# Kernel optimization log

Hardware: AMD Instinct MI355X
Metric: run time of the kernel (lower is better)

Reference implementation:

```python
import jax, jax.numpy as jnp
import numpy as np

GH = 256       # GRU hidden size
VOCAB = 1000
MAX_EP = 150
NPREV = NCURR = NNEXT = 64


def _gru_scan(emb, h0, wih, whh, bih, bhh):
    # torch nn.GRU single-layer math, scanned over the token axis
    H = h0.shape[0]
    def step(h, x_t):
        gi = wih @ x_t + bih            # [3H]
        gh = whh @ h + bhh              # [3H]
        r = jax.nn.sigmoid(gi[:H] + gh[:H])
        z = jax.nn.sigmoid(gi[H:2 * H] + gh[H:2 * H])
        n = jnp.tanh(gi[2 * H:] + r * gh[2 * H:])
        hn = (1.0 - z) * n + z * h
        return hn, hn
    _, hs = jax.lax.scan(step, h0, emb)
    return hs                            # [L, H]


def _conv(x, w, b, s):
    y = jax.lax.conv_general_dilated(x, w, (s, s), 'VALID',
                                     dimension_numbers=('NCHW', 'OIHW', 'NCHW'))
    return y + b[None, :, None, None]


def setup_inputs():
    key = jax.random.key(0)
    ks = jax.random.split(key, 48)
    f32 = jnp.float32
    def W(i, shape, s=0.05):
        return (jax.random.normal(ks[i], shape) * s).astype(f32)
    inp = dict(
        x=jax.random.normal(ks[0], (1, 3, 124, 124), f32),
        hx=jax.random.normal(ks[1], (1, 256), f32),
        cx=jax.random.normal(ks[2], (1, 256), f32),
        conv1_w=W(3, (128, 3, 8, 8)), conv1_b=jnp.zeros((128,), f32),
        conv2_w=W(4, (64, 128, 4, 4)), conv2_b=jnp.zeros((64,), f32),
        conv3_w=W(5, (64, 64, 4, 4)), conv3_b=jnp.zeros((64,), f32),
        emb_w=W(6, (VOCAB, 32), 1.0),
        gru_f_wih=W(7, (3 * GH, 32)), gru_f_whh=W(8, (3 * GH, GH)),
        gru_f_bih=jnp.zeros((3 * GH,), f32), gru_f_bhh=jnp.zeros((3 * GH,), f32),
        gru_b_wih=W(9, (3 * GH, 32)), gru_b_whh=W(10, (3 * GH, GH)),
        gru_b_bih=jnp.zeros((3 * GH,), f32), gru_b_bhh=jnp.zeros((3 * GH,), f32),
        time_emb_w=W(11, (MAX_EP + 1, 32), 1.0),
        temp_emb_w=W(12, (2, 32), 1.0),
        img_emb_w=W(13, (256, 64 * 6 * 6)), img_emb_b=jnp.zeros((256,), f32),
        attn_key_w=W(14, (256, 256 * 3)), attn_key_b=jnp.zeros((256,), f32),
        bilinear_A=W(15, (1, 256, 544)), bilinear_b=jnp.zeros((1,), f32),
        reduce_w=W(16, (128, 544)), reduce_b=jnp.zeros((128,), f32),
        gate_w=W(17, (64, 640)), gate_b=jnp.zeros((64,), f32),
        lin_w=W(18, (256, 64 * 6 * 6)), lin_b=jnp.zeros((256,), f32),
        lstm_wih=W(19, (1024, 256)), lstm_whh=W(20, (1024, 256)),
        lstm_bih=jnp.zeros((1024,), f32), lstm_bhh=jnp.zeros((1024,), f32),
        critic_w=W(21, (1, 288)), critic_b=jnp.zeros((1,), f32),
        actor_w=W(22, (4, 288)), actor_b=jnp.zeros((4,), f32),
        prev_inst=jax.random.randint(ks[23], (1, NPREV), 0, VOCAB),
        curr_inst=jax.random.randint(ks[24], (1, NCURR), 0, VOCAB),
        next_inst=jax.random.randint(ks[25], (1, NNEXT), 0, VOCAB),
        tx=jax.random.randint(ks[26], (1,), 0, MAX_EP + 1),
    )
    return inp


def reference(x, hx, cx, conv1_w, conv1_b, conv2_w, conv2_b, conv3_w, conv3_b,
              emb_w, gru_f_wih, gru_f_whh, gru_f_bih, gru_f_bhh,
              gru_b_wih, gru_b_whh, gru_b_bih, gru_b_bhh,
              time_emb_w, temp_emb_w, img_emb_w, img_emb_b,
              attn_key_w, attn_key_b, bilinear_A, bilinear_b,
              reduce_w, reduce_b, gate_w, gate_b, lin_w, lin_b,
              lstm_wih, lstm_whh, lstm_bih, lstm_bhh,
              critic_w, critic_b, actor_w, actor_b,
              prev_inst, curr_inst, next_inst, tx):
    np_, nc, nn_ = prev_inst.shape[1], curr_inst.shape[1], next_inst.shape[1]
    all_inst = jnp.concatenate([prev_inst, curr_inst, next_inst], axis=1)[0]  # [L]
    L = all_inst.shape[0]

    # CNN encoder
    h = jax.nn.relu(_conv(x, conv1_w, conv1_b, 4))
    h = jax.nn.relu(_conv(h, conv2_w, conv2_b, 2))
    x_img = jax.nn.relu(_conv(h, conv3_w, conv3_b, 2))       # [1,64,6,6]

    # token-looped GRUs -> single lax.scan each (note: original runs gru_b
    # over the SAME forward order then reverses the hidden list; replicated)
    emb = emb_w[all_inst]                                    # [L,32]
    h0 = jnp.zeros((GH,), emb.dtype)
    hs_f = _gru_scan(emb, h0, gru_f_wih, gru_f_whh, gru_f_bih, gru_f_bhh)
    hs_b = _gru_scan(emb, h0, gru_b_wih, gru_b_whh, gru_b_bih, gru_b_bhh)[::-1]
    curr_instr_rep = jnp.concatenate([hs_f[np_ + nc - 1], hs_b[np_]])[None]  # [1,512]
    ir_f = jnp.concatenate([hs_f[:np_], hs_f[L - nn_:]], axis=0)             # [M,256]
    ir_b = jnp.concatenate([hs_b[:np_], hs_b[L - nn_:]], axis=0)
    temp_tok = jnp.concatenate([jnp.zeros((np_,), jnp.int32), jnp.ones((nn_,), jnp.int32)])
    instr_rep = jnp.concatenate([ir_f, ir_b, temp_emb_w[temp_tok]], axis=1)  # [M,544]

    # bilinear attention over prev/next token states
    image_emb = x_img.reshape(1, -1) @ img_emb_w.T + img_emb_b               # [1,256]
    attn_key = jnp.concatenate([curr_instr_rep, image_emb], 1) @ attn_key_w.T + attn_key_b
    scores = jnp.einsum('k,okv,mv->mo', attn_key[0], bilinear_A, instr_rep) + bilinear_b  # [M,1]
    w = jax.nn.softmax(scores, axis=0)
    instr_sum = (instr_rep * w).sum(0, keepdims=True)                        # [1,544]

    # gating of image features
    gating = instr_sum @ reduce_w.T + reduce_b                               # [1,128]
    gate_key = jax.nn.sigmoid(jnp.concatenate([curr_instr_rep, gating], 1) @ gate_w.T + gate_b)  # [1,64]
    xg = (x_img * gate_key[:, :, None, None]).reshape(1, -1)
    z = jax.nn.relu(xg @ lin_w.T + lin_b)                                    # [1,256]

    # LSTMCell (torch gate order i,f,g,o)
    gates = z @ lstm_wih.T + lstm_bih + hx @ lstm_whh.T + lstm_bhh           # [1,1024]
    i, f, g, o = jnp.split(gates, 4, axis=1)
    cx2 = jax.nn.sigmoid(f) * cx + jax.nn.sigmoid(i) * jnp.tanh(g)
    hx2 = jax.nn.sigmoid(o) * jnp.tanh(cx2)

    feat = jnp.concatenate([hx2, time_emb_w[tx].reshape(-1, 32)], axis=1)    # [1,288]
    critic = feat @ critic_w.T + critic_b                                    # [1,1]
    actor = feat @ actor_w.T + actor_b                                       # [1,4]
    return critic, actor, hx2, cx2
```

## Files before the change

### kernel.cpp

```cpp
#include <hip/hip_runtime.h>
#include <hip/hip_bf16.h>

__device__ __forceinline__ float bf2f(unsigned short u) {
    unsigned int v = ((unsigned int)u) << 16;
    return __builtin_bit_cast(float, v);
}
__device__ __forceinline__ float sigm(float x) { return 1.0f / (1.0f + expf(-x)); }
__device__ __forceinline__ float san(float v) {
    return (v == v && fabsf(v) < 1e20f) ? v : 12345.0f;
}
__device__ __forceinline__ void wrout(void* out, int i, float v, int f32out) {
    if (f32out) ((float*)out)[i] = v;
    else ((__hip_bfloat16*)out)[i] = __float2bfloat16(v);
}
__device__ __forceinline__ int dot4(int a, int b, int c) {
#if __has_builtin(__builtin_amdgcn_sdot4)
    return __builtin_amdgcn_sdot4(a, b, c, false);
#else
    int d;
    asm("v_dot4_i32_i8 %0, %1, %2, %3" : "=v"(d) : "v"(a), "v"(b), "v"(c));
    return d;
#endif
}
__device__ __forceinline__ float fexp2(float x) {
#if __has_builtin(__builtin_amdgcn_exp2f)
    return __builtin_amdgcn_exp2f(x);
#else
    return exp2f(x);
#endif
}
__device__ __forceinline__ float frcp(float x) {
#if __has_builtin(__builtin_amdgcn_rcpf)
    return __builtin_amdgcn_rcpf(x);
#else
    return 1.0f / x;
#endif
}
__device__ __forceinline__ float fsigm(float x) {
    return frcp(1.0f + fexp2(x * -1.44269504f));
}
__device__ __forceinline__ float ftanh(float x) {
    float t = fexp2(x * 2.88539008f);
    return 1.0f - 2.0f * frcp(t + 1.0f);
}
__device__ __forceinline__ float wave_red(float acc) {
#pragma unroll
    for (int off = 32; off >= 1; off >>= 1) acc += __shfl_down(acc, off);
    return acc;
}
__device__ __forceinline__ int dpp_xor1(int a) {
    return __builtin_amdgcn_mov_dpp(a, 0xB1, 0xF, 0xF, true);
}
__device__ __forceinline__ int dpp_xor2(int a) {
    return __builtin_amdgcn_mov_dpp(a, 0x4E, 0xF, 0xF, true);
}
__device__ __forceinline__ int qsum4(int a) {
    a += dpp_xor1(a);
    a += dpp_xor2(a);
    return a;
}

struct CanonArgs {
    const void* ptr[40];
    int start[41];
    int size[40];
};

__global__ void k_flag1000(void* out) {
    if (threadIdx.x == 0) ((unsigned int*)out)[0] = 0x447A0000u;
}

__global__ void k_detect_tokens(const void* x, int nx,
                                const int* __restrict__ prev, const int* __restrict__ curr,
                                const int* __restrict__ nxt, const int* __restrict__ tx,
                                float* __restrict__ flags, int* __restrict__ toks) {
    __shared__ float sm[256];
    __shared__ int sInt64;
    int tid = threadIdx.x;
    const unsigned short* xs = (const unsigned short*)x;
    float mx = 0.0f;
    for (int i = tid; i < nx; i += 256) {
        float f = bf2f(xs[i]);
        float a = (f == f) ? fabsf(f) : 1e30f;
        mx = fmaxf(mx, a);
    }
    sm[tid] = mx;
    __syncthreads();
    for (int s = 128; s >= 1; s >>= 1) {
        if (tid < s) sm[tid] = fmaxf(sm[tid], sm[tid + s]);
        __syncthreads();
    }
    if (tid == 0) {
        flags[0] = (sm[0] > 100.0f) ? 1.0f : 0.0f;
        int anyOdd = 0;
        for (int k = 0; k < 32; ++k) anyOdd |= curr[2 * k + 1];
        int i64 = (anyOdd == 0) ? 1 : 0;
        flags[1] = (float)i64;
        sInt64 = i64;
    }
    __syncthreads();
    int stride = sInt64 ? 2 : 1;
    if (tid < 192) {
        const int* src = (tid < 64) ? prev : ((tid < 128) ? curr : nxt);
        int v = src[(tid & 63) * stride];
        toks[tid] = min(max(v, 0), 999);
    }
    if (tid == 0) toks[192] = min(max(tx[0], 0), 150);
}

__global__ void k_convert(CanonArgs a, const float* __restrict__ flags,
                          float* __restrict__ C) {
    int base = blockIdx.x << 10;
    int t = 0;
    while (t < 39 && base >= a.start[t + 1]) ++t;
    int local = base - a.start[t] + (threadIdx.x << 2);
    int sz = a.size[t];
    float4 v = make_float4(0.0f, 0.0f, 0.0f, 0.0f);
    int f32in = (flags[0] != 0.0f);
    if (local + 3 < sz) {
        if (f32in) {
            v = *(const float4*)((const float*)a.ptr[t] + local);
        } else {
            uint2 u = *(const uint2*)((const unsigned short*)a.ptr[t] + local);
            v.x = bf2f((unsigned short)(u.x & 0xffff));
            v.y = bf2f((unsigned short)(u.x >> 16));
            v.z = bf2f((unsigned short)(u.y & 0xffff));
            v.w = bf2f((unsigned short)(u.y >> 16));
        }
    } else if (local < sz) {
        float tmp[4] = {0.0f, 0.0f, 0.0f, 0.0f};
        for (int q = 0; q < 4 && local + q < sz; ++q) {
            if (f32in) tmp[q] = ((const float*)a.ptr[t])[local + q];
            else tmp[q] = bf2f(((const unsigned short*)a.ptr[t])[local + q]);
        }
        v = make_float4(tmp[0], tmp[1], tmp[2], tmp[3]);
    }
    *(float4*)(C + base + (threadIdx.x << 2)) = v;
}

__global__ void k_conv1(const float* __restrict__ x, const float* __restrict__ w,
                        const float* __restrict__ b, float* __restrict__ out) {
    int idx = blockIdx.x * 256 + threadIdx.x;
    int oc = idx / 900;
    int rem = idx - oc * 900;
    int oh = rem / 30;
    int ow = rem - oh * 30;
    float acc = b[oc];
    for (int ic = 0; ic < 3; ++ic) {
        int xb = ic * 15376 + (oh * 4) * 124 + ow * 4;
        int wb = oc * 192 + ic * 64;
#pragma unroll
        for (int kh = 0; kh < 8; ++kh) {
            const float2* xr = (const float2*)(x + xb + kh * 124);
            const float2* wr = (const float2*)(w + wb + kh * 8);
#pragma unroll
            for (int p = 0; p < 4; ++p) {
                float2 xv = xr[p];
                float2 wv = wr[p];
                acc += xv.x * wv.x + xv.y * wv.y;
            }
        }
    }
    out[idx] = fmaxf(acc, 0.0f);
}

__global__ void k_conv2(const float* __restrict__ in, const float* __restrict__ w,
                        const float* __restrict__ b, float* __restrict__ out) {
    int wid = (blockIdx.x * 256 + threadIdx.x) >> 6;
    int lane = threadIdx.x & 63;
    int oc = wid / 196;
    int rem = wid - oc * 196;
    int oh = rem / 14, ow = rem - oh * 14;
    float acc = 0.0f;
#pragma unroll 8
    for (int i = 0; i < 32; ++i) {
        int e = lane + (i << 6);
        int ic = e >> 4, k = e & 15, kh = k >> 2, kw = k & 3;
        acc += in[ic * 900 + (oh * 2 + kh) * 30 + ow * 2 + kw] * w[oc * 2048 + e];
    }
    acc = wave_red(acc);
    if (lane == 0) out[wid] = fmaxf(acc + b[oc], 0.0f);
}

__global__ void k_conv3(const float* __restrict__ in, const float* __restrict__ w,
                        const float* __restrict__ b, float* __restrict__ out) {
    int wid = (blockIdx.x * 256 + threadIdx.x) >> 6;
    int lane = threadIdx.x & 63;
    int oc = wid / 36;
    int rem = wid - oc * 36;
    int oh = rem / 6, ow = rem - oh * 6;
    float acc = 0.0f;
#pragma unroll
    for (int i = 0; i < 16; ++i) {
        int e = lane + (i << 6);
        int ic = e >> 4, k = e & 15, kh = k >> 2, kw = k & 3;
        acc += in[ic * 196 + (oh * 2 + kh) * 14 + ow * 2 + kw] * w[oc * 1024 + e];
    }
    acc = wave_red(acc);
    if (lane == 0) out[wid] = fmaxf(acc + b[oc], 0.0f);
}

__global__ void k_imgemb(const float* __restrict__ ximg, const float* __restrict__ w,
                         const float* __restrict__ b, float* __restrict__ out) {
    int j = blockIdx.x;
    int t = threadIdx.x;
    const float* wr = w + j * 2304;
    float acc = 0.0f;
    for (int k = t; k < 2304; k += 64) acc += wr[k] * ximg[k];
    acc = wave_red(acc);
    if (t == 0) out[j] = acc + b[j];
}

__global__ void k_gi(const int* __restrict__ toks, const float* __restrict__ emb,
                     const float* __restrict__ wih_f, const float* __restrict__ bih_f,
                     const float* __restrict__ bhh_f,
                     const float* __restrict__ wih_b, const float* __restrict__ bih_b,
                     const float* __restrict__ bhh_b,
                     float* __restrict__ gi) {
    int t = blockIdx.y;
    int gru = blockIdx.z;
    int j = blockIdx.x * 256 + threadIdx.x;
    __shared__ float e[32];
    int tok = toks[t];
    if (threadIdx.x < 32) e[threadIdx.x] = emb[tok * 32 + threadIdx.x];
    __syncthreads();
    const float* wih = gru ? wih_b : wih_f;
    const float* bih = gru ? bih_b : bih_f;
    const float* bhh = gru ? bhh_b : bhh_f;
    const float2* wr = (const float2*)(wih + j * 32);
    float acc = bih[j] + ((j < 512) ? bhh[j] : 0.0f);
#pragma unroll
    for (int k = 0; k < 16; ++k) {
        float2 wv = wr[k];
        acc += wv.x * e[2 * k] + wv.y * e[2 * k + 1];
    }
    gi[(gru * 192 + t) * 768 + j] = acc;
}

__global__ __launch_bounds__(512) void k_gru(
    const float* __restrict__ whh_f, const float* __restrict__ bhh_f,
    const float* __restrict__ whh_b, const float* __restrict__ bhh_b,
    const float* __restrict__ gi, float* __restrict__ hs) {
    extern __shared__ unsigned char smem[];
    unsigned int (*hq)[68] = (unsigned int (*)[68])smem;
    _Float16* hsl = (_Float16*)(smem + 1024);

    int gru = blockIdx.x;
    const float* whh = gru ? whh_b : whh_f;
    const float* bhh = gru ? bhh_b : bhh_f;
    const float* gib = gi + gru * 192 * 768;
    float* hso = hs + gru * 192 * 256;

    int t = threadIdx.x;
    int c = t & 3;
    int g = t >> 2;
    int j0 = g * 2;
    int d = c & 1;
    int jme = j0 + d;

    int wq[6][16];
    float inv[6];
#pragma unroll
    for (int rl = 0; rl < 6; ++rl) {
        int sect = rl >> 1, dd = rl & 1;
        int row = sect * 256 + j0 + dd;
        const float4* src4 = (const float4*)(whh + row * 256 + c * 64);
        float mx = 0.0f;
#pragma unroll
        for (int q = 0; q < 16; ++q) {
            float4 f = src4[q];
            mx = fmaxf(mx, fmaxf(fmaxf(fabsf(f.x), fabsf(f.y)), fmaxf(fabsf(f.z), fabsf(f.w))));
        }
        mx = fmaxf(mx, __shfl_xor(mx, 1));
        mx = fmaxf(mx, __shfl_xor(mx, 2));
        float scale = 127.0f / fmaxf(mx, 1e-20f);
        inv[rl] = mx * (1.0f / (127.0f * 127.0f));
#pragma unroll
        for (int q = 0; q < 16; ++q) {
            float4 f = src4[q];
            int p0 = (int)rintf(f.x * scale);
            int p1 = (int)rintf(f.y * scale);
            int p2 = (int)rintf(f.z * scale);
            int p3 = (int)rintf(f.w * scale);
            wq[rl][q] = (p0 & 0xff) | ((p1 & 0xff) << 8) | ((p2 & 0xff) << 16) | (p3 << 24);
        }
    }
    float bhhn = bhh[512 + jme];

    if (t < 68) {
        hq[0][t] = 0u;
        hq[1][t] = 0u;
    }
    __syncthreads();

    float hprev = 0.0f;
    float gir, giz, gin;
    {
        const float* gp = gib + jme;
        gir = gp[0]; giz = gp[256]; gin = gp[512];
    }

    for (int s = 0; s < 192; ++s) {
        int p = s & 1;
        float nir = 0.0f, niz = 0.0f, nin = 0.0f;
        if (s + 1 < 192) {
            const float* gp = gib + (s + 1) * 768 + jme;
            nir = gp[0]; niz = gp[256]; nin = gp[512];
        }
        int acc[6] = {0, 0, 0, 0, 0, 0};
        const uint4* hp = (const uint4*)&hq[p][c * 16];
#pragma unroll
        for (int blk = 0; blk < 4; ++blk) {
            uint4 hv = hp[blk];
#pragma unroll
            for (int rl = 0; rl < 6; ++rl) {
                acc[rl] = dot4(wq[rl][4 * blk + 0], (int)hv.x, acc[rl]);
                acc[rl] = dot4(wq[rl][4 * blk + 1], (int)hv.y, acc[rl]);
                acc[rl] = dot4(wq[rl][4 * blk + 2], (int)hv.z, acc[rl]);
                acc[rl] = dot4(wq[rl][4 * blk + 3], (int)hv.w, acc[rl]);
            }
        }
#pragma unroll
        for (int rl = 0; rl < 6; ++rl) acc[rl] = qsum4(acc[rl]);

        float ar = d ? (float)acc[1] * inv[1] : (float)acc[0] * inv[0];
        float az = d ? (float)acc[3] * inv[3] : (float)acc[2] * inv[2];
        float an = d ? (float)acc[5] * inv[5] : (float)acc[4] * inv[4];
        float r = fsigm(gir + ar);
        float z = fsigm(giz + az);
        float n = ftanh(gin + r * (an + bhhn));
        hprev = (1.0f - z) * n + z * hprev;

        int u = (int)(unsigned int)__builtin_bit_cast(unsigned short, (_Float16)hprev);
        int q = (int)rintf(hprev * 127.0f) & 0xff;
        int upk = u | (dpp_xor1(u) << 16);
        int qpk = q | ((dpp_xor1(q) & 0xff) << 8);
        if (c == 0) {
            ((unsigned int*)hsl)[s * 128 + g] = (unsigned int)upk;
            ((unsigned short*)&hq[1 - p][0])[g] = (unsigned short)qpk;
        }
        gir = nir; giz = niz; gin = nin;
        asm volatile("s_waitcnt lgkmcnt(0)" ::: "memory");
        __builtin_amdgcn_s_barrier();
        asm volatile("" ::: "memory");
    }

    const unsigned int* hsl32 = (const unsigned int*)hsl;
    for (int i = t; i < 24576; i += 512) {
        unsigned int u = hsl32[i];
        _Float16 lo = __builtin_bit_cast(_Float16, (unsigned short)(u & 0xffff));
        _Float16 hi = __builtin_bit_cast(_Float16, (unsigned short)(u >> 16));
        *(float2*)(hso + 2 * i) = make_float2((float)lo, (float)hi);
    }
}

__device__ __forceinline__ float ir_val(int m, int v, const float* hsf, const float* hsb,
                                        const float* temp_emb) {
    if (v < 256) { int r = (m < 64) ? m : 64 + m; return hsf[r * 256 + v]; }
    if (v < 512) { int r = (m < 64) ? 191 - m : 127 - m; return hsb[r * 256 + v - 256]; }
    return temp_emb[(m >= 64) * 32 + (v - 512)];
}

__global__ void k_attnkey(const float* __restrict__ hs, const float* __restrict__ imgemb,
                          const float* __restrict__ w, const float* __restrict__ b,
                          float* __restrict__ ak) {
    int j = blockIdx.x;
    int t = threadIdx.x;
    const float* hsf127 = hs + 127 * 256;
    const float* hsb127 = hs + 192 * 256 + 127 * 256;
    const float* wr = w + j * 768;
    float acc = 0.0f;
    for (int k = t; k < 768; k += 64) {
        float v = (k < 256) ? hsf127[k] : ((k < 512) ? hsb127[k - 256] : imgemb[k - 512]);
        acc += wr[k] * v;
    }
    acc = wave_red(acc);
    if (t == 0) ak[j] = acc + b[j];
}

__global__ void k_bilin(const float* __restrict__ A, const float* __restrict__ ak,
                        float* __restrict__ tmp) {
    int v = blockIdx.x;
    int t = threadIdx.x;
    float acc = 0.0f;
#pragma unroll
    for (int k = t; k < 256; k += 64) acc += A[k * 544 + v] * ak[k];
    acc = wave_red(acc);
    if (t == 0) tmp[v] = acc;
}

__global__ __launch_bounds__(1024) void k_attnmid(
    const float* __restrict__ hs, const float* __restrict__ temp_emb_w,
    const float* __restrict__ tmpv, const float* __restrict__ bb,
    const float* __restrict__ reduce_w, const float* __restrict__ reduce_b,
    const float* __restrict__ gate_w, const float* __restrict__ gate_b,
    float* __restrict__ gk) {
    const int tid = threadIdx.x;
    const float* hsf = hs;
    const float* hsb = hs + 192 * 256;
    __shared__ float stmp[544], ssc[128], ssum[544], sred[1024], sgating[128], scr[512];

    if (tid < 256) {
        scr[tid] = hsf[127 * 256 + tid];
        scr[256 + tid] = hsb[127 * 256 + tid];
    }
    if (tid < 544) stmp[tid] = tmpv[tid];
    __syncthreads();

    {
        int m = tid >> 3, q = tid & 7;
        float acc = 0.0f;
        for (int v = q * 68; v < q * 68 + 68; ++v) acc += stmp[v] * ir_val(m, v, hsf, hsb, temp_emb_w);
        sred[tid] = acc;
    }
    __syncthreads();
    if (tid < 128) {
        float acc = bb[0];
        for (int q = 0; q < 8; ++q) acc += sred[tid * 8 + q];
        ssc[tid] = acc;
        sred[tid] = acc;
    }
    __syncthreads();
#pragma unroll
    for (int s2 = 64; s2 >= 1; s2 >>= 1) {
        if (tid < s2) sred[tid] = fmaxf(sred[tid], sred[tid + s2]);
        __syncthreads();
    }
    float mx = sred[0];
    __syncthreads();
    if (tid < 128) {
        float e = expf(ssc[tid] - mx);
        ssc[tid] = e;
        sred[tid] = e;
    }
    __syncthreads();
#pragma unroll
    for (int s2 = 64; s2 >= 1; s2 >>= 1) {
        if (tid < s2) sred[tid] += sred[tid + s2];
        __syncthreads();
    }
    float inv = 1.0f / sred[0];
    __syncthreads();
    if (tid < 128) ssc[tid] *= inv;
    __syncthreads();

    if (tid < 544) {
        float acc = 0.0f;
        for (int m = 0; m < 128; ++m) acc += ssc[m] * ir_val(m, tid, hsf, hsb, temp_emb_w);
        ssum[tid] = acc;
    }
    __syncthreads();

    {
        int j = tid >> 3, q = tid & 7;
        const float2* wr = (const float2*)(reduce_w + j * 544 + q * 68);
        float acc = 0.0f;
        for (int k = 0; k < 34; ++k) {
            float2 wv = wr[k];
            acc += wv.x * ssum[q * 68 + 2 * k] + wv.y * ssum[q * 68 + 2 * k + 1];
        }
        sred[tid] = acc;
    }
    __syncthreads();
    if (tid < 128) {
        float acc = reduce_b[tid];
        for (int q = 0; q < 8; ++q) acc += sred[tid * 8 + q];
        sgating[tid] = acc;
    }
    __syncthreads();

    {
        int j = tid >> 4, q = tid & 15;
        const float2* wr = (const float2*)(gate_w + j * 640 + q * 40);
        float acc = 0.0f;
        for (int k = 0; k < 20; ++k) {
            float2 wv = wr[k];
            int v0 = q * 40 + 2 * k;
            float a0 = (v0 < 512) ? scr[v0] : sgating[v0 - 512];
            float a1 = (v0 + 1 < 512) ? scr[v0 + 1] : sgating[v0 + 1 - 512];
            acc += wv.x * a0 + wv.y * a1;
        }
        sred[tid] = acc;
    }
    __syncthreads();
    if (tid < 64) {
        float acc = gate_b[tid];
        for (int q = 0; q < 16; ++q) acc += sred[tid * 16 + q];
        gk[tid] = sigm(acc);
    }
}

__global__ void k_lin(const float* __restrict__ ximg, const float* __restrict__ gk,
                      const float* __restrict__ w, const float* __restrict__ b,
                      float* __restrict__ z) {
    int j = blockIdx.x;
    int t = threadIdx.x;
    __shared__ float sgk[64];
    if (t < 64) sgk[t] = gk[t];
    __syncthreads();
    const float* wr = w + j * 2304;
    float acc = 0.0f;
    for (int k = t; k < 2304; k += 64) acc += wr[k] * ximg[k] * sgk[k / 36];
    acc = wave_red(acc);
    if (t == 0) z[j] = fmaxf(acc + b[j], 0.0f);
}

__global__ void k_lstm(const float* __restrict__ z, const float* __restrict__ hx,
                       const float* __restrict__ wih, const float* __restrict__ whh,
                       const float* __restrict__ bih, const float* __restrict__ bhh,
                       float* __restrict__ sg) {
    int j = blockIdx.x;
    int t = threadIdx.x;
    const float* wi = wih + j * 256;
    const float* wh = whh + j * 256;
    float acc = 0.0f;
#pragma unroll
    for (int k = t; k < 256; k += 64) acc += wi[k] * z[k] + wh[k] * hx[k];
    acc = wave_red(acc);
    if (t == 0) sg[j] = acc + bih[j] + bhh[j];
}

__global__ __launch_bounds__(1024) void k_final(
    const float* __restrict__ sgg, const float* __restrict__ cx,
    const float* __restrict__ time_emb_w, const int* __restrict__ toks,
    const float* __restrict__ critic_w, const float* __restrict__ critic_b,
    const float* __restrict__ actor_w, const float* __restrict__ actor_b,
    const float* __restrict__ flags, void* __restrict__ out) {
    const int tid = threadIdx.x;
    __shared__ float sfeat[288], shx2[256], scx2[256], stmp[544], sred[1024];

    if (tid < 256) {
        float ii = sgg[tid], ff = sgg[256 + tid], gg = sgg[512 + tid], oo = sgg[768 + tid];
        float c2 = sigm(ff) * cx[tid] + sigm(ii) * tanhf(gg);
        float h2 = sigm(oo) * tanhf(c2);
        scx2[tid] = c2;
        shx2[tid] = h2;
        sfeat[tid] = h2;
    }
    if (tid < 32) sfeat[256 + tid] = time_emb_w[toks[192] * 32 + tid];
    __syncthreads();

    if (tid < 512) stmp[tid] = (tid < 288) ? critic_w[tid] * sfeat[tid] : 0.0f;
    {
        int a = tid >> 8, k = tid & 255;
        float pa = actor_w[a * 288 + k] * sfeat[k];
        if (k < 32) pa += actor_w[a * 288 + 256 + k] * sfeat[256 + k];
        sred[tid] = pa;
    }
    __syncthreads();
#pragma unroll
    for (int s2 = 256; s2 >= 1; s2 >>= 1) {
        if (tid < s2) stmp[tid] += stmp[tid + s2];
        int k = tid & 255;
        if (s2 <= 128 && k < s2) sred[tid] += sred[tid + s2];
        __syncthreads();
    }

    int f32out = (flags[0] != 0.0f) ? 1 : 0;
    if (tid == 0) wrout(out, 0, san(stmp[0] + critic_b[0]), f32out);
    if (tid < 4) wrout(out, 1 + tid, san(sred[tid * 256] + actor_b[tid]), f32out);
    if (tid < 256) {
        wrout(out, 5 + tid, san(shx2[tid]), f32out);
        wrout(out, 261 + tid, san(scx2[tid]), f32out);
    }
}

extern "C" void kernel_launch(void* const* d_in, const int* in_sizes, int n_in,
                              void* d_out, int out_size, void* d_ws, size_t ws_size,
                              hipStream_t stream) {
    if (n_in != 44) return;

    CanonArgs ca;
    int acc = 0;
    for (int i = 0; i < 40; ++i) {
        ca.ptr[i] = d_in[i];
        ca.start[i] = acc;
        ca.size[i] = in_sizes[i];
        acc += (in_sizes[i] + 1023) & ~1023;
    }
    ca.start[40] = acc;
    const int T = acc;

    float* ws     = (float*)d_ws;
    float* flags  = ws;
    int*   toks   = (int*)(ws + 64);
    float* imgemb = ws + 320;
    float* C      = ws + 640;
    float* gi     = C + T;
    float* hs     = gi + 294912;
    float* aux    = hs + 98304;
    float* ak     = aux;
    float* tmpv   = aux + 256;
    float* gk     = aux + 928;
    float* zv     = aux + 992;
    float* sg     = aux + 1248;
    float* h1     = gi;
    float* h2     = h1 + 115200;
    float* ximg   = h2 + 12544;

    size_t need = (size_t)(640 + T + 294912 + 98304 + 2272) * 4;
    if (ws_size < need) {
        k_flag1000<<<1, 64, 0, stream>>>(d_out);
        return;
    }

    const int* prev = (const int*)d_in[40];
    const int* curr = (const int*)d_in[41];
    const int* nxt  = (const int*)d_in[42];
    const int* tx   = (const int*)d_in[43];

    k_detect_tokens<<<1, 256, 0, stream>>>(d_in[0], in_sizes[0], prev, curr, nxt, tx,
                                           flags, toks);
    k_convert<<<T >> 10, 256, 0, stream>>>(ca, flags, C);

#define CP(i) (C + ca.start[i])
    k_gi<<<dim3(3, 192, 2), 256, 0, stream>>>(toks, CP(9),
                                              CP(10), CP(12), CP(13),
                                              CP(14), CP(16), CP(17), gi);
    k_gru<<<2, 512, 99328, stream>>>(CP(11), CP(13), CP(15), CP(17), gi, hs);
    k_conv1<<<450, 256, 0, stream>>>(CP(0), CP(3), CP(4), h1);
    k_conv2<<<3136, 256, 0, stream>>>(h1, CP(5), CP(6), h2);
    k_conv3<<<576, 256, 0, stream>>>(h2, CP(7), CP(8), ximg);
    k_imgemb<<<256, 64, 0, stream>>>(ximg, CP(20), CP(21), imgemb);
    k_attnkey<<<256, 64, 0, stream>>>(hs, imgemb, CP(22), CP(23), ak);
    k_bilin<<<544, 64, 0, stream>>>(CP(24), ak, tmpv);
    k_attnmid<<<1, 1024, 0, stream>>>(hs, CP(19), tmpv, CP(25),
                                      CP(26), CP(27), CP(28), CP(29), gk);
    k_lin<<<256, 64, 0, stream>>>(ximg, gk, CP(30), CP(31), zv);
    k_lstm<<<1024, 64, 0, stream>>>(zv, CP(1), CP(32), CP(33), CP(34), CP(35), sg);
    k_final<<<1, 1024, 0, stream>>>(sg, CP(2), CP(18), toks,
                                    CP(36), CP(37), CP(38), CP(39), flags, d_out);
#undef CP
}
```

Measured before the change: 523.4 us.

## Split GRU recurrent dot across 8 lanes with 1024 threads and store hs directly

The GRU recurrence kernel now runs 1024 threads per direction, and each group of 8 lanes splits the 256-wide hidden dot product. This halves the serial int8 dot4 chain per timestep, at the cost of one extra DPP half-mirror reduction step and a barrier across twice as many waves. The fp16 LDS staging buffer and the final copy-out loop are gone. Each step instead writes fp32 hidden states straight to global memory, which also removes the large dynamic shared allocation.

```diff
diff --git a/kernel.cpp b/kernel.cpp
--- a/kernel.cpp
+++ b/kernel.cpp
@@ -54,9 +54,13 @@
 __device__ __forceinline__ int dpp_xor2(int a) {
     return __builtin_amdgcn_mov_dpp(a, 0x4E, 0xF, 0xF, true);
 }
-__device__ __forceinline__ int qsum4(int a) {
+__device__ __forceinline__ int dpp_hmirror(int a) {
+    return __builtin_amdgcn_mov_dpp(a, 0x141, 0xF, 0xF, true);
+}
+__device__ __forceinline__ int gsum8(int a) {
     a += dpp_xor1(a);
     a += dpp_xor2(a);
+    a += dpp_hmirror(a);
     return a;
 }
 
@@ -237,13 +241,11 @@
     gi[(gru * 192 + t) * 768 + j] = acc;
 }
 
-__global__ __launch_bounds__(512) void k_gru(
+__global__ __launch_bounds__(1024, 4) void k_gru(
     const float* __restrict__ whh_f, const float* __restrict__ bhh_f,
     const float* __restrict__ whh_b, const float* __restrict__ bhh_b,
     const float* __restrict__ gi, float* __restrict__ hs) {
-    extern __shared__ unsigned char smem[];
-    unsigned int (*hq)[68] = (unsigned int (*)[68])smem;
-    _Float16* hsl = (_Float16*)(smem + 1024);
+    __shared__ unsigned int hq[2][72];
 
     int gru = blockIdx.x;
     const float* whh = gru ? whh_b : whh_f;
@@ -252,45 +254,47 @@
     float* hso = hs + gru * 192 * 256;
 
     int t = threadIdx.x;
-    int c = t & 3;
-    int g = t >> 2;
+    int c = t & 7;
+    int g = t >> 3;
     int j0 = g * 2;
     int d = c & 1;
     int jme = j0 + d;
 
-    int wq[6][16];
-    float inv[6];
+    int wq[6][8];
+    float inv6[6];
 #pragma unroll
     for (int rl = 0; rl < 6; ++rl) {
         int sect = rl >> 1, dd = rl & 1;
         int row = sect * 256 + j0 + dd;
-        const float4* src4 = (const float4*)(whh + row * 256 + c * 64);
+        const float4* src4 = (const float4*)(whh + row * 256 + c * 32);
+        float4 f[8];
         float mx = 0.0f;
 #pragma unroll
-        for (int q = 0; q < 16; ++q) {
-            float4 f = src4[q];
-            mx = fmaxf(mx, fmaxf(fmaxf(fabsf(f.x), fabsf(f.y)), fmaxf(fabsf(f.z), fabsf(f.w))));
+        for (int q = 0; q < 8; ++q) {
+            f[q] = src4[q];
+            mx = fmaxf(mx, fmaxf(fmaxf(fabsf(f[q].x), fabsf(f[q].y)),
+                                 fmaxf(fabsf(f[q].z), fabsf(f[q].w))));
         }
         mx = fmaxf(mx, __shfl_xor(mx, 1));
         mx = fmaxf(mx, __shfl_xor(mx, 2));
+        mx = fmaxf(mx, __shfl_xor(mx, 4));
         float scale = 127.0f / fmaxf(mx, 1e-20f);
-        inv[rl] = mx * (1.0f / (127.0f * 127.0f));
-#pragma unroll
-        for (int q = 0; q < 16; ++q) {
-            float4 f = src4[q];
-            int p0 = (int)rintf(f.x * scale);
-            int p1 = (int)rintf(f.y * scale);
-            int p2 = (int)rintf(f.z * scale);
-            int p3 = (int)rintf(f.w * scale);
+        inv6[rl] = mx * (1.0f / (127.0f * 127.0f));
+#pragma unroll
+        for (int q = 0; q < 8; ++q) {
+            int p0 = (int)rintf(f[q].x * scale);
+            int p1 = (int)rintf(f[q].y * scale);
+            int p2 = (int)rintf(f[q].z * scale);
+            int p3 = (int)rintf(f[q].w * scale);
             wq[rl][q] = (p0 & 0xff) | ((p1 & 0xff) << 8) | ((p2 & 0xff) << 16) | (p3 << 24);
         }
     }
+    float invR = d ? inv6[1] : inv6[0];
+    float invZ = d ? inv6[3] : inv6[2];
+    float invN = d ? inv6[5] : inv6[4];
     float bhhn = bhh[512 + jme];
 
-    if (t < 68) {
-        hq[0][t] = 0u;
-        hq[1][t] = 0u;
-    }
+    if (t < 144) ((unsigned int*)hq)[t] = 0u;
     __syncthreads();
 
     float hprev = 0.0f;
@@ -308,49 +312,48 @@
             nir = gp[0]; niz = gp[256]; nin = gp[512];
         }
         int acc[6] = {0, 0, 0, 0, 0, 0};
-        const uint4* hp = (const uint4*)&hq[p][c * 16];
-#pragma unroll
-        for (int blk = 0; blk < 4; ++blk) {
-            uint4 hv = hp[blk];
-#pragma unroll
-            for (int rl = 0; rl < 6; ++rl) {
-                acc[rl] = dot4(wq[rl][4 * blk + 0], (int)hv.x, acc[rl]);
-                acc[rl] = dot4(wq[rl][4 * blk + 1], (int)hv.y, acc[rl]);
-                acc[rl] = dot4(wq[rl][4 * blk + 2], (int)hv.z, acc[rl]);
-                acc[rl] = dot4(wq[rl][4 * blk + 3], (int)hv.w, acc[rl]);
-            }
-        }
-#pragma unroll
-        for (int rl = 0; rl < 6; ++rl) acc[rl] = qsum4(acc[rl]);
-
-        float ar = d ? (float)acc[1] * inv[1] : (float)acc[0] * inv[0];
-        float az = d ? (float)acc[3] * inv[3] : (float)acc[2] * inv[2];
-        float an = d ? (float)acc[5] * inv[5] : (float)acc[4] * inv[4];
+        const uint4* hp = (const uint4*)&hq[p][c * 8];
+        uint4 ha = hp[0];
+        uint4 hb = hp[1];
+#pragma unroll
+        for (int rl = 0; rl < 6; ++rl) {
+            acc[rl] = dot4(wq[rl][0], (int)ha.x, acc[rl]);
+            acc[rl] = dot4(wq[rl][1], (int)ha.y, acc[rl]);
+            acc[rl] = dot4(wq[rl][2], (int)ha.z, acc[rl]);
+            acc[rl] = dot4(wq[rl][3], (int)ha.w, acc[rl]);
+            acc[rl] = dot4(wq[rl][4], (int)hb.x, acc[rl]);
+            acc[rl] = dot4(wq[rl][5], (int)hb.y, acc[rl]);
+            acc[rl] = dot4(wq[rl][6], (int)hb.z, acc[rl]);
+            acc[rl] = dot4(wq[rl][7], (int)hb.w, acc[rl]);
+        }
+#pragma unroll
+        for (int rl = 0; rl < 6; ++rl) acc[rl] = gsum8(acc[rl]);
+
+        int ai_r = d ? acc[1] : acc[0];
+        int ai_z = d ? acc[3] : acc[2];
+        int ai_n = d ? acc[5] : acc[4];
+        float ar = (float)ai_r * invR;
+        float az = (float)ai_z * invZ;
+        float an = (float)ai_n * invN;
         float r = fsigm(gir + ar);
         float z = fsigm(giz + az);
         float n = ftanh(gin + r * (an + bhhn));
-        hprev = (1.0f - z) * n + z * hprev;
-
-        int u = (int)(unsigned int)__builtin_bit_cast(unsigned short, (_Float16)hprev);
+        hprev = z * (hprev - n) + n;
+
+        int hbits = __builtin_bit_cast(int, hprev);
+        int hpart = dpp_xor1(hbits);
+        if (c == 0) {
+            *(float2*)(hso + s * 256 + j0) =
+                make_float2(hprev, __builtin_bit_cast(float, hpart));
+        }
         int q = (int)rintf(hprev * 127.0f) & 0xff;
-        int upk = u | (dpp_xor1(u) << 16);
         int qpk = q | ((dpp_xor1(q) & 0xff) << 8);
-        if (c == 0) {
-            ((unsigned int*)hsl)[s * 128 + g] = (unsigned int)upk;
-            ((unsigned short*)&hq[1 - p][0])[g] = (unsigned short)qpk;
-        }
+        if (c == 0) ((unsigned short*)&hq[1 - p][0])[g] = (unsigned short)qpk;
+
         gir = nir; giz = niz; gin = nin;
         asm volatile("s_waitcnt lgkmcnt(0)" ::: "memory");
         __builtin_amdgcn_s_barrier();
         asm volatile("" ::: "memory");
-    }
-
-    const unsigned int* hsl32 = (const unsigned int*)hsl;
-    for (int i = t; i < 24576; i += 512) {
-        unsigned int u = hsl32[i];
-        _Float16 lo = __builtin_bit_cast(_Float16, (unsigned short)(u & 0xffff));
-        _Float16 hi = __builtin_bit_cast(_Float16, (unsigned short)(u >> 16));
-        *(float2*)(hso + 2 * i) = make_float2((float)lo, (float)hi);
     }
 }
 
@@ -617,7 +620,7 @@
     k_gi<<<dim3(3, 192, 2), 256, 0, stream>>>(toks, CP(9),
                                               CP(10), CP(12), CP(13),
                                               CP(14), CP(16), CP(17), gi);
-    k_gru<<<2, 512, 99328, stream>>>(CP(11), CP(13), CP(15), CP(17), gi, hs);
+    k_gru<<<2, 1024, 0, stream>>>(CP(11), CP(13), CP(15), CP(17), gi, hs);
     k_conv1<<<450, 256, 0, stream>>>(CP(0), CP(3), CP(4), h1);
     k_conv2<<<3136, 256, 0, stream>>>(h1, CP(5), CP(6), h2);
     k_conv3<<<576, 256, 0, stream>>>(h2, CP(7), CP(8), ximg);
```

Result: slower. 556.9 us (+6.4%).
